# Optimization experiments

Hardware: AMD Instinct MI355X
Metric: run time of the kernel (lower is better)

## Reference

```python
import jax, jax.numpy as jnp
import numpy as np

B, E, H, KVH, S = 1, 4096, 32, 8, 2048
HD = E // H            # per-head dim = 128
KVE = KVH * HD         # kv projection embed dim = 1024


def setup_inputs() -> dict:
    key = jax.random.key(0)
    ks = jax.random.split(key, 10)
    std = 0.02
    return {
        "input_embeds": jax.random.normal(ks[0], (B, E, 1, S), jnp.float32),
        "cos": jax.random.uniform(ks[1], (HD, S), jnp.float32, -1.0, 1.0),
        "sin": jax.random.uniform(ks[2], (HD, S), jnp.float32, -1.0, 1.0),
        "wq": jax.random.normal(ks[3], (E, E), jnp.float32) * std,
        "bq": jnp.zeros((E,), jnp.float32),
        "wk": jax.random.normal(ks[4], (KVE, E), jnp.float32) * std,
        "wv": jax.random.normal(ks[5], (KVE, E), jnp.float32) * std,
        "bv": jnp.zeros((KVE,), jnp.float32),
        "wo": jax.random.normal(ks[6], (E, E), jnp.float32) * std,
        "bo": jnp.zeros((E,), jnp.float32),
    }


def _proj(w, x, b=None):
    # 1x1 Conv2d == channelwise linear on (B, C, 1, S)
    y = jnp.einsum('oc,bcxs->boxs', w, x)
    if b is not None:
        y = y + b[None, :, None, None]
    return y


def _rope(x, cos, sin):
    # x: (B, h, HD, S); rotate-half along head_dim axis
    half = x.shape[2] // 2
    x1, x2 = x[:, :, :half], x[:, :, half:]
    rot = jnp.concatenate([-x2, x1], axis=2)
    return x * cos[None, None] + rot * sin[None, None]


def reference(input_embeds, cos, sin, wq, bq, wk, wv, bv, wo, bo):
    b, e, _, s = input_embeds.shape
    hd = e // H
    q = _proj(wq, input_embeds, bq)          # (B, E, 1, S)
    k = _proj(wk, input_embeds)              # (B, KVE, 1, S)  (no bias)
    v = _proj(wv, input_embeds, bv)          # (B, KVE, 1, S)

    qh = q.reshape(b, H, hd, s)
    kh = k.reshape(b, KVH, hd, s)
    qh = _rope(qh, cos, sin)
    kh = _rope(kh, cos, sin)

    # GQA tiling: channel-block repeat => query head h uses kv head (h % KVH)
    rep = H // KVH
    kfull = jnp.tile(kh, (1, rep, 1, 1))                       # (B, H, HD, S)
    vfull = jnp.tile(v.reshape(b, KVH, hd, s), (1, rep, 1, 1))  # (B, H, HD, S)

    scale = 1.0 / np.sqrt(hd).astype(np.float32)
    scores = jnp.einsum('bhcq,bhck->bhqk', qh, kfull) * scale  # (B, H, S, S)
    causal = jnp.tril(jnp.ones((s, s), bool))
    scores = jnp.where(causal[None, None], scores, jnp.finfo(scores.dtype).min)
    w = jax.nn.softmax(scores, axis=-1)
    attn = jnp.einsum('bhqk,bhck->bhcq', w, vfull).reshape(b, e, 1, s)
    return _proj(wo, attn, bo)
```

## Files before the change

### kernel.cpp

```cpp
#include <hip/hip_runtime.h>


typedef unsigned short u16;
typedef unsigned int u32;
typedef __attribute__((ext_vector_type(8))) short bf16x8;
typedef __attribute__((ext_vector_type(4))) float f32x4;

__device__ __forceinline__ u16 f2b(float f){
  union { float f; u32 u; } v; v.f = f;
  u32 r = (v.u + 0x7FFFu + ((v.u >> 16) & 1u)) >> 16;
  return (u16)r;
}
__device__ __forceinline__ float b2f(u16 b){
  union { u32 u; float f; } v; v.u = ((u32)b) << 16;
  return v.f;
}

__device__ __forceinline__ void gld16(const void* g, void* l){
  __builtin_amdgcn_global_load_lds((const __attribute__((address_space(1))) u32*)g,
                                   (__attribute__((address_space(3))) u32*)l, 16, 0, 0);
}

__global__ __launch_bounds__(256) void cvt_w(const float* __restrict__ src,
                                             u16* __restrict__ dst, int n4)
{
  int i = blockIdx.x * 256 + threadIdx.x;
  if (i < n4){
    float4 v = *(const float4*)&src[(size_t)i * 4];
    ushort4 o; o.x = f2b(v.x); o.y = f2b(v.y); o.z = f2b(v.z); o.w = f2b(v.w);
    *(ushort4*)&dst[(size_t)i * 4] = o;
  }
}

__global__ __launch_bounds__(256) void transpose_x(const float* __restrict__ X,
                                                   u16* __restrict__ XT)
{
  __shared__ float lds[64][65];
  const int c0 = blockIdx.x * 64, s0 = blockIdx.y * 64;
  const int tid = threadIdx.x;
  {
    const int sg = tid & 15, cl = tid >> 4;
#pragma unroll
    for (int p = 0; p < 4; ++p){
      int c = cl + p * 16;
      float4 v = *(const float4*)&X[(size_t)(c0 + c) * 2048 + s0 + sg * 4];
      lds[sg*4+0][c] = v.x; lds[sg*4+1][c] = v.y;
      lds[sg*4+2][c] = v.z; lds[sg*4+3][c] = v.w;
    }
  }
  __syncthreads();
  {
    const int cg = tid & 15, sl = tid >> 4;
#pragma unroll
    for (int p = 0; p < 4; ++p){
      int s = sl + p * 16;
      ushort4 o;
      o.x = f2b(lds[s][cg*4+0]); o.y = f2b(lds[s][cg*4+1]);
      o.z = f2b(lds[s][cg*4+2]); o.w = f2b(lds[s][cg*4+3]);
      *(ushort4*)&XT[(size_t)(s0 + s) * 4096 + c0 + cg * 4] = o;
    }
  }
}

template<int EPI, int ABF>
__global__ __launch_bounds__(256) void gemm2(
    const u16* __restrict__ W0, const u16* __restrict__ W1, const u16* __restrict__ W2,
    const float* __restrict__ F0, const float* __restrict__ F1, const float* __restrict__ F2,
    const u16* __restrict__ B,
    const float* __restrict__ bias0, const float* __restrict__ bias2,
    u16* __restrict__ QTo, u16* __restrict__ KTo, u16* __restrict__ Vno,
    float* __restrict__ OUT)
{
  const int K = 4096;
  const int m0 = blockIdx.y * 128, n0 = blockIdx.x * 128;

  const u16* A16; const float* Af; int mA;
  if (EPI == 0){
    if (m0 < 4096)      { A16 = W0; Af = F0; mA = m0; }
    else if (m0 < 5120) { A16 = W1; Af = F1; mA = m0 - 4096; }
    else                { A16 = W2; Af = F2; mA = m0 - 5120; }
  } else { A16 = W0; Af = F0; mA = m0; }

  __shared__ __align__(16) u16 As[128 * 32];
  __shared__ __align__(16) u16 Bs[128 * 32];

  const int tid = threadIdx.x, lane = tid & 63, w = tid >> 6;
  const int wm = w >> 1, wn = w & 1, quad = lane >> 4, l15 = lane & 15;

  f32x4 acc[4][4];
#pragma unroll
  for (int mt = 0; mt < 4; ++mt)
#pragma unroll
    for (int nt = 0; nt < 4; ++nt)
      acc[mt][nt] = f32x4{0.f, 0.f, 0.f, 0.f};

  const int r0 = tid >> 2, gs0 = tid & 3;
  const int g0 = gs0 ^ ((r0 >> 1) & 3);
  const int r1 = r0 + 64;

  u16* ldsA0 = As + (size_t)(w * 64) * 8;
  u16* ldsA1 = As + (size_t)(w * 64 + 256) * 8;
  u16* ldsB0 = Bs + (size_t)(w * 64) * 8;
  u16* ldsB1 = Bs + (size_t)(w * 64 + 256) * 8;

  const u16* bsrc0 = &B[(size_t)(n0 + r0) * 4096 + g0 * 8];
  const u16* bsrc1 = &B[(size_t)(n0 + r1) * 4096 + g0 * 8];
  const u16* asrc0 = ABF ? &A16[(size_t)(mA + r0) * 4096 + g0 * 8] : nullptr;
  const u16* asrc1 = ABF ? &A16[(size_t)(mA + r1) * 4096 + g0 * 8] : nullptr;
  const float* afs0 = ABF ? nullptr : &Af[(size_t)(mA + r0) * 4096 + g0 * 8];
  const float* afs1 = ABF ? nullptr : &Af[(size_t)(mA + r1) * 4096 + g0 * 8];

  int aoff[4], boff[4];
#pragma unroll
  for (int mt = 0; mt < 4; ++mt){
    int row = wm * 64 + mt * 16 + l15;
    aoff[mt] = row * 32 + (quad ^ ((row >> 1) & 3)) * 8;
  }
#pragma unroll
  for (int nt = 0; nt < 4; ++nt){
    int row = wn * 64 + nt * 16 + l15;
    boff[nt] = row * 32 + (quad ^ ((row >> 1) & 3)) * 8;
  }

  for (int kt = 0; kt < K / 32; ++kt){
    const int k0 = kt * 32;
    if (ABF){
      gld16(asrc0 + k0, ldsA0);
      gld16(asrc1 + k0, ldsA1);
    } else {
      float4 v0 = *(const float4*)&afs0[k0];
      float4 v1 = *(const float4*)&afs0[k0 + 4];
      float4 v2 = *(const float4*)&afs1[k0];
      float4 v3 = *(const float4*)&afs1[k0 + 4];
      union { u16 u[8]; uint4 q; } p0, p1;
      p0.u[0]=f2b(v0.x); p0.u[1]=f2b(v0.y); p0.u[2]=f2b(v0.z); p0.u[3]=f2b(v0.w);
      p0.u[4]=f2b(v1.x); p0.u[5]=f2b(v1.y); p0.u[6]=f2b(v1.z); p0.u[7]=f2b(v1.w);
      p1.u[0]=f2b(v2.x); p1.u[1]=f2b(v2.y); p1.u[2]=f2b(v2.z); p1.u[3]=f2b(v2.w);
      p1.u[4]=f2b(v3.x); p1.u[5]=f2b(v3.y); p1.u[6]=f2b(v3.z); p1.u[7]=f2b(v3.w);
      *(uint4*)&As[(size_t)tid * 8] = p0.q;
      *(uint4*)&As[(size_t)(tid + 256) * 8] = p1.q;
    }
    gld16(bsrc0 + k0, ldsB0);
    gld16(bsrc1 + k0, ldsB1);
    __syncthreads();

    bf16x8 af[4], bfr[4];
#pragma unroll
    for (int mt = 0; mt < 4; ++mt) af[mt]  = *(const bf16x8*)&As[aoff[mt]];
#pragma unroll
    for (int nt = 0; nt < 4; ++nt) bfr[nt] = *(const bf16x8*)&Bs[boff[nt]];
#pragma unroll
    for (int mt = 0; mt < 4; ++mt)
#pragma unroll
      for (int nt = 0; nt < 4; ++nt)
        acc[mt][nt] = __builtin_amdgcn_mfma_f32_16x16x32_bf16(af[mt], bfr[nt], acc[mt][nt], 0, 0, 0);
    __syncthreads();
  }

  if (EPI == 0){
    if (m0 < 4096){
#pragma unroll
      for (int mt = 0; mt < 4; ++mt){
        int mb = m0 + wm * 64 + mt * 16 + quad * 4;
        float b0 = bias0[mb], b1 = bias0[mb+1], b2 = bias0[mb+2], b3 = bias0[mb+3];
#pragma unroll
        for (int nt = 0; nt < 4; ++nt){
          int n = n0 + wn * 64 + nt * 16 + l15;
          ushort4 o;
          o.x = f2b(acc[mt][nt][0] + b0); o.y = f2b(acc[mt][nt][1] + b1);
          o.z = f2b(acc[mt][nt][2] + b2); o.w = f2b(acc[mt][nt][3] + b3);
          *(ushort4*)&QTo[(size_t)n * 4096 + mb] = o;
        }
      }
    } else if (m0 < 5120){
#pragma unroll
      for (int mt = 0; mt < 4; ++mt){
        int mb = m0 - 4096 + wm * 64 + mt * 16 + quad * 4;
#pragma unroll
        for (int nt = 0; nt < 4; ++nt){
          int n = n0 + wn * 64 + nt * 16 + l15;
          ushort4 o;
          o.x = f2b(acc[mt][nt][0]); o.y = f2b(acc[mt][nt][1]);
          o.z = f2b(acc[mt][nt][2]); o.w = f2b(acc[mt][nt][3]);
          *(ushort4*)&KTo[(size_t)n * 1024 + mb] = o;
        }
      }
    } else {
#pragma unroll
      for (int mt = 0; mt < 4; ++mt)
#pragma unroll
        for (int r = 0; r < 4; ++r){
          int mv = m0 - 5120 + wm * 64 + mt * 16 + quad * 4 + r;
          float bb = bias2[mv];
#pragma unroll
          for (int nt = 0; nt < 4; ++nt){
            int n = n0 + wn * 64 + nt * 16 + l15;
            Vno[(size_t)mv * 2048 + n] = f2b(acc[mt][nt][r] + bb);
          }
        }
    }
  } else {
#pragma unroll
    for (int mt = 0; mt < 4; ++mt)
#pragma unroll
      for (int r = 0; r < 4; ++r){
        int m = m0 + wm * 64 + mt * 16 + quad * 4 + r;
        float bb = bias0[m];
#pragma unroll
        for (int nt = 0; nt < 4; ++nt){
          int n = n0 + wn * 64 + nt * 16 + l15;
          OUT[(size_t)m * 2048 + n] = acc[mt][nt][r] + bb;
        }
      }
  }
}

template<int EPI>
__global__ __launch_bounds__(512, 2) void gemm256(
    const u16* __restrict__ W0, const u16* __restrict__ W1, const u16* __restrict__ W2,
    const u16* __restrict__ Bmat,
    const float* __restrict__ bias0, const float* __restrict__ bias2,
    u16* __restrict__ QTo, u16* __restrict__ KTo, u16* __restrict__ Vno,
    float* __restrict__ OUT)
{
  const int NT = 64;
  const int m0 = blockIdx.y * 256, n0 = blockIdx.x * 256;

  const u16* A16; int mA;
  if (EPI == 0){
    if (m0 < 4096)      { A16 = W0; mA = m0; }
    else if (m0 < 5120) { A16 = W1; mA = m0 - 4096; }
    else                { A16 = W2; mA = m0 - 5120; }
  } else { A16 = W0; mA = m0; }

  __shared__ __align__(16) u16 As[2 * 2 * 8192];
  __shared__ __align__(16) u16 Bs[2 * 2 * 8192];

  const int tid = threadIdx.x, lane = tid & 63, w = tid >> 6;
  const int wm = w >> 2, wn = w & 3, quad = lane >> 4, l15 = lane & 15;

  f32x4 acc[8][4];
#pragma unroll
  for (int mt = 0; mt < 8; ++mt)
#pragma unroll
    for (int nt = 0; nt < 4; ++nt)
      acc[mt][nt] = f32x4{0.f, 0.f, 0.f, 0.f};

  const int rowq = tid >> 2;
  const int kg   = (tid & 3) * 8;
  const u16* aG = &A16[(size_t)(mA + rowq) * 4096 + kg];
  const u16* bG = &Bmat[(size_t)(n0 + rowq) * 4096 + kg];
  u16* AsW = As + w * 512;
  u16* BsW = Bs + w * 512;

  int aoff[8], boff[4];
#pragma unroll
  for (int mt = 0; mt < 8; ++mt) aoff[mt] = (wm * 128 + mt * 16 + l15) * 32 + quad * 8;
#pragma unroll
  for (int nt = 0; nt < 4; ++nt) boff[nt] = (wn * 64 + nt * 16 + l15) * 32 + quad * 8;

  auto stage8 = [&](int b, int k0){
    u16* Ad = AsW + b * 16384;
    u16* Bd = BsW + b * 16384;
    const u16* as_ = aG + k0;
    const u16* bs_ = bG + k0;
    gld16(as_,                   Ad);
    gld16(as_ + 128 * 4096,      Ad + 4096);
    gld16(bs_,                   Bd);
    gld16(bs_ + 128 * 4096,      Bd + 4096);
    gld16(as_ + 32,              Ad + 8192);
    gld16(as_ + 32 + 128 * 4096, Ad + 8192 + 4096);
    gld16(bs_ + 32,              Bd + 8192);
    gld16(bs_ + 32 + 128 * 4096, Bd + 8192 + 4096);
  };

  stage8(0, 0);
  asm volatile("s_waitcnt vmcnt(4)" ::: "memory");
  __builtin_amdgcn_s_barrier();
  __builtin_amdgcn_sched_barrier(0);

#pragma unroll 1
  for (int t = 0; t < NT; ++t){
    const int buf = t & 1;
    const u16* Asl = As + buf * 16384;
    const u16* Bsl = Bs + buf * 16384;

    {
      bf16x8 af[8], bf[4];
#pragma unroll
      for (int mt = 0; mt < 8; ++mt) af[mt] = *(const bf16x8*)&Asl[aoff[mt]];
#pragma unroll
      for (int nt = 0; nt < 4; ++nt) bf[nt] = *(const bf16x8*)&Bsl[boff[nt]];
      if (t + 1 < NT) stage8((t + 1) & 1, (t + 1) * 64);
      __builtin_amdgcn_s_setprio(1);
#pragma unroll
      for (int mt = 0; mt < 8; ++mt)
#pragma unroll
        for (int nt = 0; nt < 4; ++nt)
          acc[mt][nt] = __builtin_amdgcn_mfma_f32_16x16x32_bf16(af[mt], bf[nt], acc[mt][nt], 0, 0, 0);
      __builtin_amdgcn_s_setprio(0);
      if (t + 1 < NT) { asm volatile("s_waitcnt vmcnt(8)" ::: "memory"); }
      else            { asm volatile("s_waitcnt vmcnt(0)" ::: "memory"); }
      __builtin_amdgcn_s_barrier();
      __builtin_amdgcn_sched_barrier(0);
    }
    {
      bf16x8 af[8], bf[4];
#pragma unroll
      for (int mt = 0; mt < 8; ++mt) af[mt] = *(const bf16x8*)&Asl[8192 + aoff[mt]];
#pragma unroll
      for (int nt = 0; nt < 4; ++nt) bf[nt] = *(const bf16x8*)&Bsl[8192 + boff[nt]];
      __builtin_amdgcn_s_setprio(1);
#pragma unroll
      for (int mt = 0; mt < 8; ++mt)
#pragma unroll
        for (int nt = 0; nt < 4; ++nt)
          acc[mt][nt] = __builtin_amdgcn_mfma_f32_16x16x32_bf16(af[mt], bf[nt], acc[mt][nt], 0, 0, 0);
      __builtin_amdgcn_s_setprio(0);
      if (t + 1 < NT) { asm volatile("s_waitcnt vmcnt(4)" ::: "memory"); }
      __builtin_amdgcn_s_barrier();
      __builtin_amdgcn_sched_barrier(0);
    }
  }

  if (EPI == 0){
    if (m0 < 4096){
#pragma unroll
      for (int mt = 0; mt < 8; ++mt){
        int mb = m0 + wm * 128 + mt * 16 + quad * 4;
        float b0 = bias0[mb], b1 = bias0[mb+1], b2 = bias0[mb+2], b3 = bias0[mb+3];
#pragma unroll
        for (int nt = 0; nt < 4; ++nt){
          int n = n0 + wn * 64 + nt * 16 + l15;
          ushort4 o;
          o.x = f2b(acc[mt][nt][0] + b0); o.y = f2b(acc[mt][nt][1] + b1);
          o.z = f2b(acc[mt][nt][2] + b2); o.w = f2b(acc[mt][nt][3] + b3);
          *(ushort4*)&QTo[(size_t)n * 4096 + mb] = o;
        }
      }
    } else if (m0 < 5120){
#pragma unroll
      for (int mt = 0; mt < 8; ++mt){
        int mb = m0 - 4096 + wm * 128 + mt * 16 + quad * 4;
#pragma unroll
        for (int nt = 0; nt < 4; ++nt){
          int n = n0 + wn * 64 + nt * 16 + l15;
          ushort4 o;
          o.x = f2b(acc[mt][nt][0]); o.y = f2b(acc[mt][nt][1]);
          o.z = f2b(acc[mt][nt][2]); o.w = f2b(acc[mt][nt][3]);
          *(ushort4*)&KTo[(size_t)n * 1024 + mb] = o;
        }
      }
    } else {
#pragma unroll
      for (int mt = 0; mt < 8; ++mt)
#pragma unroll
        for (int r = 0; r < 4; ++r){
          int mv = m0 - 5120 + wm * 128 + mt * 16 + quad * 4 + r;
          float bb = bias2[mv];
#pragma unroll
          for (int nt = 0; nt < 4; ++nt){
            int n = n0 + wn * 64 + nt * 16 + l15;
            Vno[(size_t)mv * 2048 + n] = f2b(acc[mt][nt][r] + bb);
          }
        }
    }
  } else {
#pragma unroll
    for (int mt = 0; mt < 8; ++mt)
#pragma unroll
      for (int r = 0; r < 4; ++r){
        int m = m0 + wm * 128 + mt * 16 + quad * 4 + r;
        float bb = bias0[m];
#pragma unroll
        for (int nt = 0; nt < 4; ++nt){
          int n = n0 + wn * 64 + nt * 16 + l15;
          OUT[(size_t)m * 2048 + n] = acc[mt][nt][r] + bb;
        }
      }
  }
}

__global__ __launch_bounds__(256) void rope_kernel(u16* __restrict__ QT,
                                                   u16* __restrict__ KT,
                                                   const float* __restrict__ cosp,
                                                   const float* __restrict__ sinp)
{
  const float qscale = 0.08838834764831845f * 1.4426950408889634f;
  int gid = blockIdx.x * 256 + threadIdx.x;
  const int NQ = 2048 * 32 * 64;
  if (gid < NQ){
    int c = gid & 63, hh = (gid >> 6) & 31, s = gid >> 11;
    size_t base = (size_t)s * 4096 + hh * 128 + c;
    float x1 = b2f(QT[base]), x2 = b2f(QT[base + 64]);
    float c1 = cosp[c * 2048 + s],        s1 = sinp[c * 2048 + s];
    float c2 = cosp[(c + 64) * 2048 + s], s2 = sinp[(c + 64) * 2048 + s];
    QT[base]      = f2b((x1 * c1 - x2 * s1) * qscale);
    QT[base + 64] = f2b((x2 * c2 + x1 * s2) * qscale);
  } else {
    int g = gid - NQ;
    int c = g & 63, hh = (g >> 6) & 7, s = g >> 9;
    size_t base = (size_t)s * 1024 + hh * 128 + c;
    float x1 = b2f(KT[base]), x2 = b2f(KT[base + 64]);
    float c1 = cosp[c * 2048 + s],        s1 = sinp[c * 2048 + s];
    float c2 = cosp[(c + 64) * 2048 + s], s2 = sinp[(c + 64) * 2048 + s];
    KT[base]      = f2b(x1 * c1 - x2 * s1);
    KT[base + 64] = f2b(x2 * c2 + x1 * s2);
  }
}

__global__ __launch_bounds__(256, 1) void attn4(const u16* __restrict__ QT,
                                                const u16* __restrict__ KT,
                                                const u16* __restrict__ Vn,
                                                u16* __restrict__ AT)
{
  const int h = blockIdx.x;
  const int Y = blockIdx.y;
  const int q = (Y < 8) ? Y : 23 - Y;
  const int kvh = h & 7;
  const int tid = threadIdx.x;
  const int w = tid >> 6, lane = tid & 63;
  const int quad = lane >> 4, l15 = lane & 15;

  const int t = (w < 2) ? (2 * q + w) : (62 - 2 * q + (w - 2));
  const int e  = t >> 1;
  const int i0 = t * 32;
  const int U  = 32 - q;

  __shared__ __align__(16) u16 Ks[2][64 * 128];
  __shared__ __align__(16) u16 Vs[128 * 64];
  __shared__ __align__(16) u16 Ps[4][16][64];

  bf16x8 qa[2][4];
#pragma unroll
  for (int mt = 0; mt < 2; ++mt)
#pragma unroll
    for (int kc = 0; kc < 4; ++kc)
      qa[mt][kc] = *(const bf16x8*)&QT[(size_t)(i0 + mt * 16 + l15) * 4096
                                       + h * 128 + kc * 32 + quad * 8];

  f32x4 o[2][9];
#pragma unroll
  for (int mt = 0; mt < 2; ++mt)
#pragma unroll
    for (int ct = 0; ct < 9; ++ct)
      o[mt][ct] = f32x4{0.f, 0.f, 0.f, 0.f};

  bf16x8 ones;
#pragma unroll
  for (int z = 0; z < 8; ++z) ones[z] = (short)0x3F80;

  const int krl = lane >> 4, kgl = lane & 15;
  const int vrl = lane >> 3, vgl = lane & 7;

  auto stageK = [&](int buf, int j0){
#pragma unroll
    for (int qq = 0; qq < 4; ++qq){
      int r = w * 16 + qq * 4 + krl;
      gld16(&KT[(size_t)(j0 + r) * 1024 + kvh * 128 + ((kgl ^ (r & 7)) * 8)],
            &Ks[buf][(size_t)(w * 16 + qq * 4) * 128]);
    }
  };
  auto stageV = [&](int j0){
#pragma unroll
    for (int qq = 0; qq < 4; ++qq){
      int r = w * 32 + qq * 8 + vrl;
      gld16(&Vn[(size_t)(kvh * 128 + r) * 2048 + j0 + ((vgl ^ (r & 7)) * 8)],
            &Vs[(size_t)(w * 32 + qq * 8) * 64]);
    }
  };

  stageK(0, 0);
  for (int u = 0; u < U; ++u){
    __syncthreads();
    if (u + 1 < U) stageK((u + 1) & 1, (u + 1) * 64);
    stageV(u * 64);

    const int j0 = u * 64;
    const bool act = (u <= e);
    const u16* Kb = &Ks[u & 1][0];

    f32x4 s[2][4];
    bf16x8 pa[2][2];
    if (act){
#pragma unroll
      for (int mt = 0; mt < 2; ++mt)
#pragma unroll
        for (int nt = 0; nt < 4; ++nt)
          s[mt][nt] = f32x4{0.f, 0.f, 0.f, 0.f};
#pragma unroll
      for (int nt = 0; nt < 4; ++nt){
        bf16x8 kb[4];
#pragma unroll
        for (int kc = 0; kc < 4; ++kc){
          int row = nt * 16 + l15;
          kb[kc] = *(const bf16x8*)&Kb[row * 128 + (((kc * 4 + quad) ^ (row & 7)) * 8)];
        }
#pragma unroll
        for (int kc = 0; kc < 4; ++kc){
          s[0][nt] = __builtin_amdgcn_mfma_f32_16x16x32_bf16(qa[0][kc], kb[kc], s[0][nt], 0, 0, 0);
          s[1][nt] = __builtin_amdgcn_mfma_f32_16x16x32_bf16(qa[1][kc], kb[kc], s[1][nt], 0, 0, 0);
        }
      }
      const bool maskit = (u == e);
#pragma unroll
      for (int mt = 0; mt < 2; ++mt){
#pragma unroll
        for (int nt = 0; nt < 4; ++nt)
#pragma unroll
          for (int r = 0; r < 4; ++r){
            float pv = exp2f(fminf(s[mt][nt][r], 60.0f));
            if (maskit && (j0 + nt * 16 + l15 > i0 + mt * 16 + quad * 4 + r)) pv = 0.0f;
            int col = nt * 16 + l15, rowp = quad * 4 + r;
            Ps[w][rowp][((col >> 3) ^ (rowp & 7)) * 8 + (col & 7)] = f2b(pv);
          }
#pragma unroll
        for (int kc = 0; kc < 2; ++kc){
          pa[mt][kc] = *(const bf16x8*)&Ps[w][l15][((kc * 4 + quad) ^ (l15 & 7)) * 8];
          o[mt][8] = __builtin_amdgcn_mfma_f32_16x16x32_bf16(pa[mt][kc], ones, o[mt][8], 0, 0, 0);
        }
      }
    }
    __syncthreads();

    if (act){
#pragma unroll
      for (int ct = 0; ct < 8; ++ct)
#pragma unroll
        for (int kc = 0; kc < 2; ++kc){
          int row = ct * 16 + l15;
          bf16x8 vb = *(const bf16x8*)&Vs[row * 64 + (((kc * 4 + quad) ^ (row & 7)) * 8)];
          o[0][ct] = __builtin_amdgcn_mfma_f32_16x16x32_bf16(pa[0][kc], vb, o[0][ct], 0, 0, 0);
          o[1][ct] = __builtin_amdgcn_mfma_f32_16x16x32_bf16(pa[1][kc], vb, o[1][ct], 0, 0, 0);
        }
      if (u == e){
#pragma unroll
        for (int mt = 0; mt < 2; ++mt){
          float rinv[4];
#pragma unroll
          for (int r = 0; r < 4; ++r) rinv[r] = 1.0f / o[mt][8][r];
#pragma unroll
          for (int ct = 0; ct < 8; ++ct)
#pragma unroll
            for (int r = 0; r < 4; ++r){
              int i = i0 + mt * 16 + quad * 4 + r;
              AT[(size_t)i * 4096 + h * 128 + ct * 16 + l15] = f2b(o[mt][ct][r] * rinv[r]);
            }
        }
      }
    }
  }
}

extern "C" void kernel_launch(void* const* d_in, const int* in_sizes, int n_in,
                              void* d_out, int out_size, void* d_ws, size_t ws_size,
                              hipStream_t stream)
{
  const float* X    = (const float*)d_in[0];
  const float* cosp = (const float*)d_in[1];
  const float* sinp = (const float*)d_in[2];
  const float* wq   = (const float*)d_in[3];
  const float* bq   = (const float*)d_in[4];
  const float* wk   = (const float*)d_in[5];
  const float* wv   = (const float*)d_in[6];
  const float* bv   = (const float*)d_in[7];
  const float* wo   = (const float*)d_in[8];
  const float* bo   = (const float*)d_in[9];
  float* out = (float*)d_out;

  char* ws = (char*)d_ws;
  const size_t MB = 1u << 20;

  if (ws_size >= 88 * MB){
    u16* W16Q = (u16*)(ws);
    u16* W16K = (u16*)(ws + 32 * MB);
    u16* W16V = (u16*)(ws + 40 * MB);
    u16* XT   = (u16*)(ws + 48 * MB);
    u16* QT   = (u16*)(ws + 64 * MB);
    u16* KT   = (u16*)(ws + 80 * MB);
    u16* Vn   = (u16*)(ws + 84 * MB);
    u16* AT   = (u16*)(ws + 48 * MB);
    u16* WO16 = (u16*)(ws);

    cvt_w<<<16384, 256, 0, stream>>>(wq, W16Q, 4194304);
    cvt_w<<< 4096, 256, 0, stream>>>(wk, W16K, 1048576);
    cvt_w<<< 4096, 256, 0, stream>>>(wv, W16V, 1048576);
    transpose_x<<<dim3(64, 32), 256, 0, stream>>>(X, XT);
    gemm256<0><<<dim3(8, 24), 512, 0, stream>>>(W16Q, W16K, W16V, XT,
                                                bq, bv, QT, KT, Vn, nullptr);
    cvt_w<<<16384, 256, 0, stream>>>(wo, WO16, 4194304);
    rope_kernel<<<20480, 256, 0, stream>>>(QT, KT, cosp, sinp);
    attn4<<<dim3(32, 16), 256, 0, stream>>>(QT, KT, Vn, AT);
    gemm256<1><<<dim3(8, 16), 512, 0, stream>>>(WO16, nullptr, nullptr, AT,
                                                bo, nullptr, nullptr, nullptr, nullptr, out);
  } else {
    u16* XT = (u16*)(ws);
    u16* QT = (u16*)(ws + 16 * MB);
    u16* KT = (u16*)(ws + 32 * MB);
    u16* Vn = (u16*)(ws + 36 * MB);
    u16* AT = (u16*)(ws + 40 * MB);

    transpose_x<<<dim3(64, 32), 256, 0, stream>>>(X, XT);
    gemm2<0,0><<<dim3(16, 48), 256, 0, stream>>>(nullptr, nullptr, nullptr, wq, wk, wv,
                                                 XT, bq, bv, QT, KT, Vn, nullptr);
    rope_kernel<<<20480, 256, 0, stream>>>(QT, KT, cosp, sinp);
    attn4<<<dim3(32, 16), 256, 0, stream>>>(QT, KT, Vn, AT);
    gemm2<1,0><<<dim3(16, 32), 256, 0, stream>>>(nullptr, nullptr, nullptr, wo, nullptr, nullptr,
                                                 AT, bo, nullptr, nullptr, nullptr, nullptr, out);
  }
}
```

Measured before the change: 676.9 us.

## Rework attention into 512-thread blocks and add BM-templated GEMM with LDS swizzle

The attention kernel now uses 8 waves per block, each taking a contiguous 32-row query tile with per-group key-length bounds. This replaces the old paired front/back load-balancing scheme and halves the grid height. It also adds explicit vmcnt waits instead of a full syncthreads, reorders the V staging, and raises wave priority around the MFMA calls. The GEMM gains a BM template parameter so the output projection runs with 128-row tiles and twice as many blocks, plus an XOR swizzle on LDS addresses to reduce bank conflicts. The risks are load imbalance across groups with different causal lengths and wrong hand-tuned vmcnt counts.

```diff
diff --git a/kernel.cpp b/kernel.cpp
--- a/kernel.cpp
+++ b/kernel.cpp
@@ -215,7 +215,7 @@
   }
 }
 
-template<int EPI>
+template<int EPI, int BM>
 __global__ __launch_bounds__(512, 2) void gemm256(
     const u16* __restrict__ W0, const u16* __restrict__ W1, const u16* __restrict__ W2,
     const u16* __restrict__ Bmat,
@@ -224,7 +224,11 @@
     float* __restrict__ OUT)
 {
   const int NT = 64;
-  const int m0 = blockIdx.y * 256, n0 = blockIdx.x * 256;
+  const int m0 = blockIdx.y * BM, n0 = blockIdx.x * 256;
+  constexpr int MT    = BM / 32;
+  constexpr int ACH   = BM / 128;
+  constexpr int SLICE = BM * 32;
+  constexpr int ABUF  = 2 * SLICE;
 
   const u16* A16; int mA;
   if (EPI == 0){
@@ -233,91 +237,105 @@
     else                { A16 = W2; mA = m0 - 5120; }
   } else { A16 = W0; mA = m0; }
 
-  __shared__ __align__(16) u16 As[2 * 2 * 8192];
+  __shared__ __align__(16) u16 As[2 * ABUF];
   __shared__ __align__(16) u16 Bs[2 * 2 * 8192];
 
   const int tid = threadIdx.x, lane = tid & 63, w = tid >> 6;
   const int wm = w >> 2, wn = w & 3, quad = lane >> 4, l15 = lane & 15;
 
-  f32x4 acc[8][4];
-#pragma unroll
-  for (int mt = 0; mt < 8; ++mt)
+  f32x4 acc[MT][4];
+#pragma unroll
+  for (int mt = 0; mt < MT; ++mt)
 #pragma unroll
     for (int nt = 0; nt < 4; ++nt)
       acc[mt][nt] = f32x4{0.f, 0.f, 0.f, 0.f};
 
   const int rowq = tid >> 2;
-  const int kg   = (tid & 3) * 8;
-  const u16* aG = &A16[(size_t)(mA + rowq) * 4096 + kg];
-  const u16* bG = &Bmat[(size_t)(n0 + rowq) * 4096 + kg];
+  const int kgA  = ((tid & 3) ^ ((rowq >> 1) & 3)) * 8;
+  const u16* aG = &A16[(size_t)(mA + rowq) * 4096 + kgA];
+  const u16* bG = &Bmat[(size_t)(n0 + rowq) * 4096 + kgA];
   u16* AsW = As + w * 512;
   u16* BsW = Bs + w * 512;
 
-  int aoff[8], boff[4];
-#pragma unroll
-  for (int mt = 0; mt < 8; ++mt) aoff[mt] = (wm * 128 + mt * 16 + l15) * 32 + quad * 8;
-#pragma unroll
-  for (int nt = 0; nt < 4; ++nt) boff[nt] = (wn * 64 + nt * 16 + l15) * 32 + quad * 8;
-
-  auto stage8 = [&](int b, int k0){
-    u16* Ad = AsW + b * 16384;
+  int aoff[MT], boff[4];
+#pragma unroll
+  for (int mt = 0; mt < MT; ++mt){
+    int row = wm * (BM / 2) + mt * 16 + l15;
+    aoff[mt] = row * 32 + ((quad ^ ((row >> 1) & 3)) * 8);
+  }
+#pragma unroll
+  for (int nt = 0; nt < 4; ++nt){
+    int row = wn * 64 + nt * 16 + l15;
+    boff[nt] = row * 32 + ((quad ^ ((row >> 1) & 3)) * 8);
+  }
+
+  auto stageT = [&](int b, int k0){
+    u16* Ad = AsW + b * ABUF;
     u16* Bd = BsW + b * 16384;
     const u16* as_ = aG + k0;
     const u16* bs_ = bG + k0;
-    gld16(as_,                   Ad);
-    gld16(as_ + 128 * 4096,      Ad + 4096);
-    gld16(bs_,                   Bd);
-    gld16(bs_ + 128 * 4096,      Bd + 4096);
-    gld16(as_ + 32,              Ad + 8192);
-    gld16(as_ + 32 + 128 * 4096, Ad + 8192 + 4096);
-    gld16(bs_ + 32,              Bd + 8192);
+    gld16(as_, Ad);
+    if constexpr (ACH == 2) gld16(as_ + 128 * 4096, Ad + 4096);
+    gld16(bs_, Bd);
+    gld16(bs_ + 128 * 4096, Bd + 4096);
+    gld16(as_ + 32, Ad + SLICE);
+    if constexpr (ACH == 2) gld16(as_ + 32 + 128 * 4096, Ad + SLICE + 4096);
+    gld16(bs_ + 32, Bd + 8192);
     gld16(bs_ + 32 + 128 * 4096, Bd + 8192 + 4096);
   };
 
-  stage8(0, 0);
-  asm volatile("s_waitcnt vmcnt(4)" ::: "memory");
+  stageT(0, 0);
+  if constexpr (BM == 256) asm volatile("s_waitcnt vmcnt(4)" ::: "memory");
+  else                     asm volatile("s_waitcnt vmcnt(3)" ::: "memory");
   __builtin_amdgcn_s_barrier();
   __builtin_amdgcn_sched_barrier(0);
 
 #pragma unroll 1
   for (int t = 0; t < NT; ++t){
     const int buf = t & 1;
-    const u16* Asl = As + buf * 16384;
+    const u16* Asl = As + buf * ABUF;
     const u16* Bsl = Bs + buf * 16384;
 
     {
-      bf16x8 af[8], bf[4];
-#pragma unroll
-      for (int mt = 0; mt < 8; ++mt) af[mt] = *(const bf16x8*)&Asl[aoff[mt]];
+      bf16x8 af[MT], bf[4];
+#pragma unroll
+      for (int mt = 0; mt < MT; ++mt) af[mt] = *(const bf16x8*)&Asl[aoff[mt]];
 #pragma unroll
       for (int nt = 0; nt < 4; ++nt) bf[nt] = *(const bf16x8*)&Bsl[boff[nt]];
-      if (t + 1 < NT) stage8((t + 1) & 1, (t + 1) * 64);
+      if (t + 1 < NT) stageT((t + 1) & 1, (t + 1) * 64);
       __builtin_amdgcn_s_setprio(1);
 #pragma unroll
-      for (int mt = 0; mt < 8; ++mt)
+      for (int mt = 0; mt < MT; ++mt)
 #pragma unroll
         for (int nt = 0; nt < 4; ++nt)
           acc[mt][nt] = __builtin_amdgcn_mfma_f32_16x16x32_bf16(af[mt], bf[nt], acc[mt][nt], 0, 0, 0);
       __builtin_amdgcn_s_setprio(0);
-      if (t + 1 < NT) { asm volatile("s_waitcnt vmcnt(8)" ::: "memory"); }
-      else            { asm volatile("s_waitcnt vmcnt(0)" ::: "memory"); }
+      if (t + 1 < NT){
+        if constexpr (BM == 256) asm volatile("s_waitcnt vmcnt(8)" ::: "memory");
+        else                     asm volatile("s_waitcnt vmcnt(6)" ::: "memory");
+      } else {
+        asm volatile("s_waitcnt vmcnt(0)" ::: "memory");
+      }
       __builtin_amdgcn_s_barrier();
       __builtin_amdgcn_sched_barrier(0);
     }
     {
-      bf16x8 af[8], bf[4];
-#pragma unroll
-      for (int mt = 0; mt < 8; ++mt) af[mt] = *(const bf16x8*)&Asl[8192 + aoff[mt]];
+      bf16x8 af[MT], bf[4];
+#pragma unroll
+      for (int mt = 0; mt < MT; ++mt) af[mt] = *(const bf16x8*)&Asl[SLICE + aoff[mt]];
 #pragma unroll
       for (int nt = 0; nt < 4; ++nt) bf[nt] = *(const bf16x8*)&Bsl[8192 + boff[nt]];
       __builtin_amdgcn_s_setprio(1);
 #pragma unroll
-      for (int mt = 0; mt < 8; ++mt)
+      for (int mt = 0; mt < MT; ++mt)
 #pragma unroll
         for (int nt = 0; nt < 4; ++nt)
           acc[mt][nt] = __builtin_amdgcn_mfma_f32_16x16x32_bf16(af[mt], bf[nt], acc[mt][nt], 0, 0, 0);
       __builtin_amdgcn_s_setprio(0);
-      if (t + 1 < NT) { asm volatile("s_waitcnt vmcnt(4)" ::: "memory"); }
+      if (t + 1 < NT){
+        if constexpr (BM == 256) asm volatile("s_waitcnt vmcnt(4)" ::: "memory");
+        else                     asm volatile("s_waitcnt vmcnt(3)" ::: "memory");
+      }
       __builtin_amdgcn_s_barrier();
       __builtin_amdgcn_sched_barrier(0);
     }
@@ -326,8 +344,8 @@
   if (EPI == 0){
     if (m0 < 4096){
 #pragma unroll
-      for (int mt = 0; mt < 8; ++mt){
-        int mb = m0 + wm * 128 + mt * 16 + quad * 4;
+      for (int mt = 0; mt < MT; ++mt){
+        int mb = m0 + wm * (BM / 2) + mt * 16 + quad * 4;
         float b0 = bias0[mb], b1 = bias0[mb+1], b2 = bias0[mb+2], b3 = bias0[mb+3];
 #pragma unroll
         for (int nt = 0; nt < 4; ++nt){
@@ -340,8 +358,8 @@
       }
     } else if (m0 < 5120){
 #pragma unroll
-      for (int mt = 0; mt < 8; ++mt){
-        int mb = m0 - 4096 + wm * 128 + mt * 16 + quad * 4;
+      for (int mt = 0; mt < MT; ++mt){
+        int mb = m0 - 4096 + wm * (BM / 2) + mt * 16 + quad * 4;
 #pragma unroll
         for (int nt = 0; nt < 4; ++nt){
           int n = n0 + wn * 64 + nt * 16 + l15;
@@ -353,10 +371,10 @@
       }
     } else {
 #pragma unroll
-      for (int mt = 0; mt < 8; ++mt)
+      for (int mt = 0; mt < MT; ++mt)
 #pragma unroll
         for (int r = 0; r < 4; ++r){
-          int mv = m0 - 5120 + wm * 128 + mt * 16 + quad * 4 + r;
+          int mv = m0 - 5120 + wm * (BM / 2) + mt * 16 + quad * 4 + r;
           float bb = bias2[mv];
 #pragma unroll
           for (int nt = 0; nt < 4; ++nt){
@@ -367,10 +385,10 @@
     }
   } else {
 #pragma unroll
-    for (int mt = 0; mt < 8; ++mt)
+    for (int mt = 0; mt < MT; ++mt)
 #pragma unroll
       for (int r = 0; r < 4; ++r){
-        int m = m0 + wm * 128 + mt * 16 + quad * 4 + r;
+        int m = m0 + wm * (BM / 2) + mt * 16 + quad * 4 + r;
         float bb = bias0[m];
 #pragma unroll
         for (int nt = 0; nt < 4; ++nt){
@@ -409,27 +427,26 @@
   }
 }
 
-__global__ __launch_bounds__(256, 1) void attn4(const u16* __restrict__ QT,
+__global__ __launch_bounds__(512, 2) void attn5(const u16* __restrict__ QT,
                                                 const u16* __restrict__ KT,
                                                 const u16* __restrict__ Vn,
                                                 u16* __restrict__ AT)
 {
   const int h = blockIdx.x;
-  const int Y = blockIdx.y;
-  const int q = (Y < 8) ? Y : 23 - Y;
+  const int g = blockIdx.y;
   const int kvh = h & 7;
   const int tid = threadIdx.x;
   const int w = tid >> 6, lane = tid & 63;
   const int quad = lane >> 4, l15 = lane & 15;
 
-  const int t = (w < 2) ? (2 * q + w) : (62 - 2 * q + (w - 2));
-  const int e  = t >> 1;
+  const int t = 8 * g + w;
+  const int e = t >> 1;
   const int i0 = t * 32;
-  const int U  = 32 - q;
+  const int U = 4 * g + 4;
 
   __shared__ __align__(16) u16 Ks[2][64 * 128];
   __shared__ __align__(16) u16 Vs[128 * 64];
-  __shared__ __align__(16) u16 Ps[4][16][64];
+  __shared__ __align__(16) u16 Ps[8][16][64];
 
   bf16x8 qa[2][4];
 #pragma unroll
@@ -455,26 +472,26 @@
 
   auto stageK = [&](int buf, int j0){
 #pragma unroll
-    for (int qq = 0; qq < 4; ++qq){
-      int r = w * 16 + qq * 4 + krl;
+    for (int qq = 0; qq < 2; ++qq){
+      int r = w * 8 + qq * 4 + krl;
       gld16(&KT[(size_t)(j0 + r) * 1024 + kvh * 128 + ((kgl ^ (r & 7)) * 8)],
-            &Ks[buf][(size_t)(w * 16 + qq * 4) * 128]);
+            &Ks[buf][(size_t)(w * 8 + qq * 4) * 128]);
     }
   };
   auto stageV = [&](int j0){
 #pragma unroll
-    for (int qq = 0; qq < 4; ++qq){
-      int r = w * 32 + qq * 8 + vrl;
+    for (int qq = 0; qq < 2; ++qq){
+      int r = w * 16 + qq * 8 + vrl;
       gld16(&Vn[(size_t)(kvh * 128 + r) * 2048 + j0 + ((vgl ^ (r & 7)) * 8)],
-            &Vs[(size_t)(w * 32 + qq * 8) * 64]);
+            &Vs[(size_t)(w * 16 + qq * 8) * 64]);
     }
   };
 
   stageK(0, 0);
   for (int u = 0; u < U; ++u){
     __syncthreads();
+    stageV(u * 64);
     if (u + 1 < U) stageK((u + 1) & 1, (u + 1) * 64);
-    stageV(u * 64);
 
     const int j0 = u * 64;
     const bool act = (u <= e);
@@ -496,11 +513,13 @@
           int row = nt * 16 + l15;
           kb[kc] = *(const bf16x8*)&Kb[row * 128 + (((kc * 4 + quad) ^ (row & 7)) * 8)];
         }
+        __builtin_amdgcn_s_setprio(1);
 #pragma unroll
         for (int kc = 0; kc < 4; ++kc){
           s[0][nt] = __builtin_amdgcn_mfma_f32_16x16x32_bf16(qa[0][kc], kb[kc], s[0][nt], 0, 0, 0);
           s[1][nt] = __builtin_amdgcn_mfma_f32_16x16x32_bf16(qa[1][kc], kb[kc], s[1][nt], 0, 0, 0);
         }
+        __builtin_amdgcn_s_setprio(0);
       }
       const bool maskit = (u == e);
 #pragma unroll
@@ -521,18 +540,24 @@
         }
       }
     }
-    __syncthreads();
+    if (u + 1 < U) asm volatile("s_waitcnt vmcnt(2)" ::: "memory");
+    else           asm volatile("s_waitcnt vmcnt(0)" ::: "memory");
+    __builtin_amdgcn_s_barrier();
+    __builtin_amdgcn_sched_barrier(0);
 
     if (act){
 #pragma unroll
-      for (int ct = 0; ct < 8; ++ct)
+      for (int ct = 0; ct < 8; ++ct){
 #pragma unroll
         for (int kc = 0; kc < 2; ++kc){
           int row = ct * 16 + l15;
           bf16x8 vb = *(const bf16x8*)&Vs[row * 64 + (((kc * 4 + quad) ^ (row & 7)) * 8)];
+          __builtin_amdgcn_s_setprio(1);
           o[0][ct] = __builtin_amdgcn_mfma_f32_16x16x32_bf16(pa[0][kc], vb, o[0][ct], 0, 0, 0);
           o[1][ct] = __builtin_amdgcn_mfma_f32_16x16x32_bf16(pa[1][kc], vb, o[1][ct], 0, 0, 0);
-        }
+          __builtin_amdgcn_s_setprio(0);
+        }
+      }
       if (u == e){
 #pragma unroll
         for (int mt = 0; mt < 2; ++mt){
@@ -586,13 +611,13 @@
     cvt_w<<< 4096, 256, 0, stream>>>(wk, W16K, 1048576);
     cvt_w<<< 4096, 256, 0, stream>>>(wv, W16V, 1048576);
     transpose_x<<<dim3(64, 32), 256, 0, stream>>>(X, XT);
-    gemm256<0><<<dim3(8, 24), 512, 0, stream>>>(W16Q, W16K, W16V, XT,
-                                                bq, bv, QT, KT, Vn, nullptr);
+    gemm256<0, 256><<<dim3(8, 24), 512, 0, stream>>>(W16Q, W16K, W16V, XT,
+                                                     bq, bv, QT, KT, Vn, nullptr);
     cvt_w<<<16384, 256, 0, stream>>>(wo, WO16, 4194304);
     rope_kernel<<<20480, 256, 0, stream>>>(QT, KT, cosp, sinp);
-    attn4<<<dim3(32, 16), 256, 0, stream>>>(QT, KT, Vn, AT);
-    gemm256<1><<<dim3(8, 16), 512, 0, stream>>>(WO16, nullptr, nullptr, AT,
-                                                bo, nullptr, nullptr, nullptr, nullptr, out);
+    attn5<<<dim3(32, 8), 512, 0, stream>>>(QT, KT, Vn, AT);
+    gemm256<1, 128><<<dim3(8, 32), 512, 0, stream>>>(WO16, nullptr, nullptr, AT,
+                                                     bo, nullptr, nullptr, nullptr, nullptr, out);
   } else {
     u16* XT = (u16*)(ws);
     u16* QT = (u16*)(ws + 16 * MB);
@@ -604,7 +629,7 @@
     gemm2<0,0><<<dim3(16, 48), 256, 0, stream>>>(nullptr, nullptr, nullptr, wq, wk, wv,
                                                  XT, bq, bv, QT, KT, Vn, nullptr);
     rope_kernel<<<20480, 256, 0, stream>>>(QT, KT, cosp, sinp);
-    attn4<<<dim3(32, 16), 256, 0, stream>>>(QT, KT, Vn, AT);
+    attn5<<<dim3(32, 8), 512, 0, stream>>>(QT, KT, Vn, AT);
     gemm2<1,0><<<dim3(16, 32), 256, 0, stream>>>(nullptr, nullptr, nullptr, wo, nullptr, nullptr,
                                                  AT, bo, nullptr, nullptr, nullptr, nullptr, out);
   }
```

Measured after the change: 598.5 us. -11.6%, faster.
